# Optimization experiments

Measured on AMD Instinct MI355X. Metric: run time of the kernel, lower is better.

Reference implementation:

```python
import jax, jax.numpy as jnp
import numpy as np

B, S, D, H = 4, 2048, 1024, 16
HD = D // H

def setup_inputs() -> dict:
    key = jax.random.key(0)
    ks = jax.random.split(key, 9)
    s = 1.0 / np.sqrt(D)
    return {
        "x": jax.random.normal(ks[0], (B, S, D), dtype=jnp.float32),
        "wq": jax.random.normal(ks[1], (D, D), dtype=jnp.float32) * s,
        "bq": jnp.zeros((D,), dtype=jnp.float32),
        "wk": jax.random.normal(ks[2], (D, D), dtype=jnp.float32) * s,
        "bk": jnp.zeros((D,), dtype=jnp.float32),
        "wv": jax.random.normal(ks[3], (D, D), dtype=jnp.float32) * s,
        "bv": jnp.zeros((D,), dtype=jnp.float32),
        "wo": jax.random.normal(ks[4], (D, D), dtype=jnp.float32) * s,
        "bo": jnp.zeros((D,), dtype=jnp.float32),
    }

def reference(x, wq, bq, wk, bk, wv, bv, wo, bo):
    # QKV projections, split heads: [B,S,D] -> [B,H,S,HD]
    def split_heads(t):
        return t.reshape(B, S, H, HD).transpose(0, 2, 1, 3)
    q = split_heads(x @ wq + bq)
    k = split_heads(x @ wk + bk)
    v = split_heads(x @ wv + bv)
    # scaled dot-product attention with full score matrix [B,H,S,S]
    scores = jnp.einsum("bhqd,bhkd->bhqk", q, k) / jnp.sqrt(jnp.float32(HD))
    weights = jax.nn.softmax(scores, axis=-1)
    attn = jnp.einsum("bhqk,bhkd->bhqd", weights, v)
    # merge heads and output projection
    out = attn.transpose(0, 2, 1, 3).reshape(B, S, D) @ wo + bo
    return out
```

## Files before the change

kernel.cpp:

```cpp
#include <hip/hip_runtime.h>
#include <hip/hip_bf16.h>


#define B_  4
#define S_  2048
#define D_  1024
#define H_  16
#define HD_ 64
#define M_  (B_*S_)

typedef __attribute__((ext_vector_type(8))) short short8;
typedef __attribute__((ext_vector_type(4))) float f32x4;
typedef __hip_bfloat16 bf16;

__device__ inline void gload_lds16(const void* g, void* l) {
  __builtin_amdgcn_global_load_lds(
      (const __attribute__((address_space(1))) void*)g,
      (__attribute__((address_space(3))) void*)l,
      16, 0, 0);
}

__device__ inline f32x4 mfma16(short8 a, short8 b, f32x4 c) {
  return __builtin_amdgcn_mfma_f32_16x16x32_bf16(a, b, c, 0, 0, 0);
}

__device__ inline short bfbits(float f) {
  bf16 h = (bf16)f;
  return *reinterpret_cast<short*>(&h);
}

__global__ void convert_x_kernel(const float* __restrict__ x, bf16* __restrict__ xb) {
  const int i = (blockIdx.x * 256 + threadIdx.x) * 8;
  float4 a = *reinterpret_cast<const float4*>(x + i);
  float4 b = *reinterpret_cast<const float4*>(x + i + 4);
  bf16 o[8];
  o[0] = (bf16)a.x; o[1] = (bf16)a.y; o[2] = (bf16)a.z; o[3] = (bf16)a.w;
  o[4] = (bf16)b.x; o[5] = (bf16)b.y; o[6] = (bf16)b.z; o[7] = (bf16)b.w;
  *reinterpret_cast<int4*>(xb + i) = *reinterpret_cast<const int4*>(o);
}

struct TP { const float* w[4]; bf16* wt[4]; };

__global__ void transpose_w_kernel(TP p) {
  const float* w = p.w[blockIdx.z];
  bf16* wt = p.wt[blockIdx.z];
  __shared__ float t[32][33];
  const int k0 = blockIdx.y * 32, n0 = blockIdx.x * 32;
  const int c = threadIdx.x & 31, r4 = threadIdx.x >> 5;
  #pragma unroll
  for (int i = 0; i < 4; ++i) {
    int r = r4 + i * 8;
    t[r][c] = w[(size_t)(k0 + r) * D_ + n0 + c];
  }
  __syncthreads();
  #pragma unroll
  for (int i = 0; i < 4; ++i) {
    int r = r4 + i * 8;
    wt[(size_t)(n0 + r) * D_ + k0 + c] = (bf16)t[c][r];
  }
}

template<int MODE>
__global__ __launch_bounds__(256) void gemm_kernel(
    const bf16* __restrict__ A, const bf16* __restrict__ Bt,
    const float* __restrict__ bias, void* __restrict__ out, float alpha)
{
  constexpr int BK = 32;
  __shared__ __align__(16) bf16 As[128 * BK];
  __shared__ __align__(16) bf16 Bs[128 * BK];
  const int tid = threadIdx.x;
  const int w = tid >> 6, l = tid & 63;
  const int lo = l & 15, hi = l >> 4;
  const int wm = w >> 1, wn = w & 1;
  const int row0 = blockIdx.y * 128;
  const int col0 = blockIdx.x * 128;

  f32x4 acc[4][4] = {};

  for (int kt = 0; kt < D_; kt += BK) {
    __syncthreads();
    #pragma unroll
    for (int i = 0; i < 2; ++i) {
      const int cb = i * 256 + w * 64;
      const int c  = cb + l;
      gload_lds16(A  + (size_t)(row0 + (c >> 2)) * D_ + kt + (c & 3) * 8,
                  (void*)(As + cb * 8));
      gload_lds16(Bt + (size_t)(col0 + (c >> 2)) * D_ + kt + (c & 3) * 8,
                  (void*)(Bs + cb * 8));
    }
    __syncthreads();

    short8 a[4], b[4];
    #pragma unroll
    for (int m = 0; m < 4; ++m)
      a[m] = *reinterpret_cast<const short8*>(As + (wm*64 + m*16 + lo) * BK + hi*8);
    #pragma unroll
    for (int n = 0; n < 4; ++n)
      b[n] = *reinterpret_cast<const short8*>(Bs + (wn*64 + n*16 + lo) * BK + hi*8);
    #pragma unroll
    for (int m = 0; m < 4; ++m)
      #pragma unroll
      for (int n = 0; n < 4; ++n)
        acc[m][n] = mfma16(a[m], b[n], acc[m][n]);
  }

  #pragma unroll
  for (int n = 0; n < 4; ++n) {
    const int c = col0 + wn*64 + n*16 + lo;
    const float bv = bias[c];
    #pragma unroll
    for (int m = 0; m < 4; ++m) {
      #pragma unroll
      for (int j = 0; j < 4; ++j) {
        const int r = row0 + wm*64 + m*16 + hi*4 + j;
        const float v = (acc[m][n][j] + bv) * alpha;
        if (MODE == 2) {
          ((float*)out)[(size_t)r * D_ + c] = v;
        } else {
          const int bb = r >> 11, s = r & (S_ - 1);
          const int h = c >> 6, hd = c & 63;
          bf16* o = (bf16*)out;
          if (MODE == 0)
            o[((size_t)(bb * H_ + h) * S_ + s) * HD_ + hd] = (bf16)v;
          else
            o[((size_t)(bb * H_ + h) * HD_ + hd) * S_ + s] = (bf16)v;
        }
      }
    }
  }
}

__global__ __launch_bounds__(256, 2) void attn_kernel(
    const bf16* __restrict__ q, const bf16* __restrict__ k,
    const bf16* __restrict__ vt, bf16* __restrict__ ao)
{
  __shared__ __align__(16) bf16 Kl[64 * 72];
  __shared__ __align__(16) bf16 Vtl[64 * 72];

  const int tid = threadIdx.x;
  const int w = tid >> 6, l = tid & 63;
  const int lo = l & 15, hi = l >> 4;
  const int bh = blockIdx.y;
  const int q0 = blockIdx.x * 256 + w * 64;

  const bf16* kbase = k  + (size_t)bh * S_ * HD_;
  const bf16* vbase = vt + (size_t)bh * HD_ * S_;

  short8 bq[4][2];
  const size_t qrow = (size_t)bh * S_ + q0;
  #pragma unroll
  for (int n = 0; n < 4; ++n)
    #pragma unroll
    for (int kk = 0; kk < 2; ++kk)
      bq[n][kk] = *reinterpret_cast<const short8*>(
          q + (qrow + n*16 + lo) * HD_ + kk*32 + hi*8);

  f32x4 o[4][4] = {};
  float mrun[4], lrun[4];
  #pragma unroll
  for (int n = 0; n < 4; ++n) { mrun[n] = -3.0e38f; lrun[n] = 0.0f; }

  const int r0 = tid >> 3,        co0 = (tid & 7) * 8;
  const int r1 = (tid + 256) >> 3, co1 = (tid & 7) * 8;

  int4 kreg0, kreg1, vreg0, vreg1;
  kreg0 = *reinterpret_cast<const int4*>(kbase + (size_t)r0 * HD_ + co0);
  kreg1 = *reinterpret_cast<const int4*>(kbase + (size_t)r1 * HD_ + co1);
  vreg0 = *reinterpret_cast<const int4*>(vbase + (size_t)r0 * S_ + co0);
  vreg1 = *reinterpret_cast<const int4*>(vbase + (size_t)r1 * S_ + co1);

  for (int kt = 0; kt < S_; kt += 64) {
    __syncthreads();
    *reinterpret_cast<int4*>(Kl  + r0*72 + co0) = kreg0;
    *reinterpret_cast<int4*>(Kl  + r1*72 + co1) = kreg1;
    *reinterpret_cast<int4*>(Vtl + r0*72 + co0) = vreg0;
    *reinterpret_cast<int4*>(Vtl + r1*72 + co1) = vreg1;
    if (kt + 64 < S_) {
      const int nt = kt + 64;
      kreg0 = *reinterpret_cast<const int4*>(kbase + (size_t)(nt + r0) * HD_ + co0);
      kreg1 = *reinterpret_cast<const int4*>(kbase + (size_t)(nt + r1) * HD_ + co1);
      vreg0 = *reinterpret_cast<const int4*>(vbase + (size_t)r0 * S_ + nt + co0);
      vreg1 = *reinterpret_cast<const int4*>(vbase + (size_t)r1 * S_ + nt + co1);
    }
    __syncthreads();

    f32x4 s[4][4] = {};
    __builtin_amdgcn_s_setprio(1);
    #pragma unroll
    for (int m = 0; m < 4; ++m) {
      short8 kf0 = *reinterpret_cast<const short8*>(Kl + (m*16+lo)*72 + hi*8);
      short8 kf1 = *reinterpret_cast<const short8*>(Kl + (m*16+lo)*72 + 32 + hi*8);
      #pragma unroll
      for (int n = 0; n < 4; ++n) {
        s[m][n] = mfma16(kf0, bq[n][0], s[m][n]);
        s[m][n] = mfma16(kf1, bq[n][1], s[m][n]);
      }
    }
    __builtin_amdgcn_s_setprio(0);

    short8 pb[4][2];
    #pragma unroll
    for (int n = 0; n < 4; ++n) {
      float mx = fmaxf(
          fmaxf(fmaxf(fmaxf(s[0][n][0], s[0][n][1]), fmaxf(s[0][n][2], s[0][n][3])),
                fmaxf(fmaxf(s[1][n][0], s[1][n][1]), fmaxf(s[1][n][2], s[1][n][3]))),
          fmaxf(fmaxf(fmaxf(s[2][n][0], s[2][n][1]), fmaxf(s[2][n][2], s[2][n][3])),
                fmaxf(fmaxf(s[3][n][0], s[3][n][1]), fmaxf(s[3][n][2], s[3][n][3]))));
      mx = fmaxf(mx, __shfl_xor(mx, 16, 64));
      mx = fmaxf(mx, __shfl_xor(mx, 32, 64));
      const float mn = fmaxf(mrun[n], mx);
      const float corr = __expf(mrun[n] - mn);
      mrun[n] = mn;
      float sum = 0.0f;
      #pragma unroll
      for (int m = 0; m < 4; ++m)
        #pragma unroll
        for (int j = 0; j < 4; ++j) {
          const float p = __expf(s[m][n][j] - mn);
          s[m][n][j] = p;
          sum += p;
        }
      sum += __shfl_xor(sum, 16, 64);
      sum += __shfl_xor(sum, 32, 64);
      lrun[n] = lrun[n] * corr + sum;
      #pragma unroll
      for (int mm = 0; mm < 4; ++mm)
        #pragma unroll
        for (int j = 0; j < 4; ++j)
          o[mm][n][j] *= corr;
      #pragma unroll
      for (int kk = 0; kk < 2; ++kk) {
        short8 t;
        t[0] = bfbits(s[2*kk][n][0]);   t[1] = bfbits(s[2*kk][n][1]);
        t[2] = bfbits(s[2*kk][n][2]);   t[3] = bfbits(s[2*kk][n][3]);
        t[4] = bfbits(s[2*kk+1][n][0]); t[5] = bfbits(s[2*kk+1][n][1]);
        t[6] = bfbits(s[2*kk+1][n][2]); t[7] = bfbits(s[2*kk+1][n][3]);
        pb[n][kk] = t;
      }
    }

    __builtin_amdgcn_s_setprio(1);
    #pragma unroll
    for (int mm = 0; mm < 4; ++mm) {
      short8 vf[2];
      #pragma unroll
      for (int kk = 0; kk < 2; ++kk) {
        union { short8 v; uint2 u2[2]; } x;
        x.u2[0] = *reinterpret_cast<const uint2*>(Vtl + (mm*16+lo)*72 + kk*32 + hi*4);
        x.u2[1] = *reinterpret_cast<const uint2*>(Vtl + (mm*16+lo)*72 + kk*32 + 16 + hi*4);
        vf[kk] = x.v;
      }
      #pragma unroll
      for (int n = 0; n < 4; ++n) {
        o[mm][n] = mfma16(vf[0], pb[n][0], o[mm][n]);
        o[mm][n] = mfma16(vf[1], pb[n][1], o[mm][n]);
      }
    }
    __builtin_amdgcn_s_setprio(0);
  }

  const int b = bh >> 4, h = bh & 15;
  #pragma unroll
  for (int n = 0; n < 4; ++n) {
    const float inv = 1.0f / lrun[n];
    const size_t row = (size_t)b * S_ + q0 + n*16 + lo;
    #pragma unroll
    for (int mm = 0; mm < 4; ++mm) {
      bf16 ov[4];
      #pragma unroll
      for (int j = 0; j < 4; ++j) ov[j] = (bf16)(o[mm][n][j] * inv);
      *reinterpret_cast<uint2*>(ao + row * D_ + h*64 + mm*16 + hi*4) =
          *reinterpret_cast<const uint2*>(ov);
    }
  }
}

extern "C" void kernel_launch(void* const* d_in, const int* in_sizes, int n_in,
                              void* d_out, int out_size, void* d_ws, size_t ws_size,
                              hipStream_t stream) {
  const float* x  = (const float*)d_in[0];
  const float* wq = (const float*)d_in[1];
  const float* bq = (const float*)d_in[2];
  const float* wk = (const float*)d_in[3];
  const float* bk = (const float*)d_in[4];
  const float* wv = (const float*)d_in[5];
  const float* bv = (const float*)d_in[6];
  const float* wo = (const float*)d_in[7];
  const float* bo = (const float*)d_in[8];

  char* ws = (char*)d_ws;
  bf16* xb  = (bf16*)(ws);
  bf16* wqt = (bf16*)(ws + ((size_t)16 << 20));
  bf16* wkt = (bf16*)(ws + ((size_t)18 << 20));
  bf16* wvt = (bf16*)(ws + ((size_t)20 << 20));
  bf16* wot = (bf16*)(ws + ((size_t)22 << 20));
  bf16* qb  = (bf16*)(ws + ((size_t)24 << 20));
  bf16* kb  = (bf16*)(ws + ((size_t)40 << 20));
  bf16* vtb = (bf16*)(ws + ((size_t)56 << 20));
  bf16* aob = (bf16*)(ws + ((size_t)72 << 20));

  convert_x_kernel<<<dim3((M_ * D_) / (256 * 8)), 256, 0, stream>>>(x, xb);

  TP p;
  p.w[0] = wq; p.w[1] = wk; p.w[2] = wv; p.w[3] = wo;
  p.wt[0] = wqt; p.wt[1] = wkt; p.wt[2] = wvt; p.wt[3] = wot;
  transpose_w_kernel<<<dim3(32, 32, 4), 256, 0, stream>>>(p);

  dim3 ggrid(D_ / 128, M_ / 128);
  gemm_kernel<0><<<ggrid, 256, 0, stream>>>(xb, wqt, bq, qb, 0.125f);
  gemm_kernel<0><<<ggrid, 256, 0, stream>>>(xb, wkt, bk, kb, 1.0f);
  gemm_kernel<1><<<ggrid, 256, 0, stream>>>(xb, wvt, bv, vtb, 1.0f);

  attn_kernel<<<dim3(S_ / 256, B_ * H_), 256, 0, stream>>>(qb, kb, vtb, aob);

  gemm_kernel<2><<<ggrid, 256, 0, stream>>>(aob, wot, bo, d_out, 1.0f);
}
```

Baseline: 323.8 us.

## Fuse QKV GEMMs, shrink attention tiles, add lazy softmax rescale and exp2

Replaces the three separate Q/K/V projection GEMMs with one launch over the concatenated transposed weights, which happen to be laid out contiguously in the workspace. Each output column is routed to the Q, K or V layout in the epilogue. The attention kernel now gives each wave 32 query rows instead of 64, allows 4 blocks per CU, and remaps the flat block index to group blocks by head. It also folds log2(e) into the Q scale so it can use exp2, and skips the rescale of the output accumulator unless the running max grows by more than 8. The output GEMM uses 64-row tiles so the grid has more blocks. The costs are fewer MFMAs per K/V tile load, bounded growth of unnormalised probabilities, and a dependence on the workspace layout.

```diff
diff --git a/kernel.cpp b/kernel.cpp
--- a/kernel.cpp
+++ b/kernel.cpp
@@ -8,6 +8,7 @@
 #define H_  16
 #define HD_ 64
 #define M_  (B_*S_)
+#define QSCALE (0.125f * 1.4426950408889634f)
 
 typedef __attribute__((ext_vector_type(8))) short short8;
 typedef __attribute__((ext_vector_type(4))) float f32x4;
@@ -60,10 +61,11 @@
   }
 }
 
-template<int MODE>
-__global__ __launch_bounds__(256) void gemm_kernel(
-    const bf16* __restrict__ A, const bf16* __restrict__ Bt,
-    const float* __restrict__ bias, void* __restrict__ out, float alpha)
+__global__ __launch_bounds__(256) void gemm_qkv_kernel(
+    const bf16* __restrict__ A, const bf16* __restrict__ Bt3,
+    const float* __restrict__ bq, const float* __restrict__ bk,
+    const float* __restrict__ bv,
+    bf16* __restrict__ qb, bf16* __restrict__ kb, bf16* __restrict__ vtb)
 {
   constexpr int BK = 32;
   __shared__ __align__(16) bf16 As[128 * BK];
@@ -83,22 +85,94 @@
     for (int i = 0; i < 2; ++i) {
       const int cb = i * 256 + w * 64;
       const int c  = cb + l;
-      gload_lds16(A  + (size_t)(row0 + (c >> 2)) * D_ + kt + (c & 3) * 8,
+      gload_lds16(A   + (size_t)(row0 + (c >> 2)) * D_ + kt + (c & 3) * 8,
                   (void*)(As + cb * 8));
+      gload_lds16(Bt3 + (size_t)(col0 + (c >> 2)) * D_ + kt + (c & 3) * 8,
+                  (void*)(Bs + cb * 8));
+    }
+    __syncthreads();
+
+    short8 a[4], b[4];
+    #pragma unroll
+    for (int m = 0; m < 4; ++m)
+      a[m] = *reinterpret_cast<const short8*>(As + (wm*64 + m*16 + lo) * BK + hi*8);
+    #pragma unroll
+    for (int n = 0; n < 4; ++n)
+      b[n] = *reinterpret_cast<const short8*>(Bs + (wn*64 + n*16 + lo) * BK + hi*8);
+    #pragma unroll
+    for (int m = 0; m < 4; ++m)
+      #pragma unroll
+      for (int n = 0; n < 4; ++n)
+        acc[m][n] = mfma16(a[m], b[n], acc[m][n]);
+  }
+
+  #pragma unroll
+  for (int n = 0; n < 4; ++n) {
+    const int c3 = col0 + wn*64 + n*16 + lo;
+    const int which = c3 >> 10;
+    const int cc = c3 & 1023;
+    const int h = cc >> 6, hd = cc & 63;
+    const float* bias = (which == 0) ? bq : (which == 1) ? bk : bv;
+    const float bvv = bias[cc];
+    #pragma unroll
+    for (int m = 0; m < 4; ++m) {
+      #pragma unroll
+      for (int j = 0; j < 4; ++j) {
+        const int r = row0 + wm*64 + m*16 + hi*4 + j;
+        const int bb = r >> 11, s = r & (S_ - 1);
+        float v = acc[m][n][j] + bvv;
+        if (which == 0) {
+          v *= QSCALE;
+          qb[((size_t)(bb * H_ + h) * S_ + s) * HD_ + hd] = (bf16)v;
+        } else if (which == 1) {
+          kb[((size_t)(bb * H_ + h) * S_ + s) * HD_ + hd] = (bf16)v;
+        } else {
+          vtb[((size_t)(bb * H_ + h) * HD_ + hd) * S_ + s] = (bf16)v;
+        }
+      }
+    }
+  }
+}
+
+__global__ __launch_bounds__(256) void gemm_out_kernel(
+    const bf16* __restrict__ A, const bf16* __restrict__ Bt,
+    const float* __restrict__ bias, float* __restrict__ out)
+{
+  constexpr int BK = 32;
+  __shared__ __align__(16) bf16 As[64 * BK];
+  __shared__ __align__(16) bf16 Bs[128 * BK];
+  const int tid = threadIdx.x;
+  const int w = tid >> 6, l = tid & 63;
+  const int lo = l & 15, hi = l >> 4;
+  const int wm = w >> 1, wn = w & 1;
+  const int row0 = blockIdx.y * 64;
+  const int col0 = blockIdx.x * 128;
+
+  f32x4 acc[2][4] = {};
+
+  for (int kt = 0; kt < D_; kt += BK) {
+    __syncthreads();
+    #pragma unroll
+    for (int i = 0; i < 2; ++i) {
+      const int cb = i * 256 + w * 64;
+      const int c  = cb + l;
+      if (i == 0)
+        gload_lds16(A + (size_t)(row0 + (c >> 2)) * D_ + kt + (c & 3) * 8,
+                    (void*)(As + cb * 8));
       gload_lds16(Bt + (size_t)(col0 + (c >> 2)) * D_ + kt + (c & 3) * 8,
                   (void*)(Bs + cb * 8));
     }
     __syncthreads();
 
-    short8 a[4], b[4];
-    #pragma unroll
-    for (int m = 0; m < 4; ++m)
-      a[m] = *reinterpret_cast<const short8*>(As + (wm*64 + m*16 + lo) * BK + hi*8);
+    short8 a[2], b[4];
+    #pragma unroll
+    for (int m = 0; m < 2; ++m)
+      a[m] = *reinterpret_cast<const short8*>(As + (wm*32 + m*16 + lo) * BK + hi*8);
     #pragma unroll
     for (int n = 0; n < 4; ++n)
       b[n] = *reinterpret_cast<const short8*>(Bs + (wn*64 + n*16 + lo) * BK + hi*8);
     #pragma unroll
-    for (int m = 0; m < 4; ++m)
+    for (int m = 0; m < 2; ++m)
       #pragma unroll
       for (int n = 0; n < 4; ++n)
         acc[m][n] = mfma16(a[m], b[n], acc[m][n]);
@@ -107,30 +181,19 @@
   #pragma unroll
   for (int n = 0; n < 4; ++n) {
     const int c = col0 + wn*64 + n*16 + lo;
-    const float bv = bias[c];
-    #pragma unroll
-    for (int m = 0; m < 4; ++m) {
+    const float bvv = bias[c];
+    #pragma unroll
+    for (int m = 0; m < 2; ++m) {
       #pragma unroll
       for (int j = 0; j < 4; ++j) {
-        const int r = row0 + wm*64 + m*16 + hi*4 + j;
-        const float v = (acc[m][n][j] + bv) * alpha;
-        if (MODE == 2) {
-          ((float*)out)[(size_t)r * D_ + c] = v;
-        } else {
-          const int bb = r >> 11, s = r & (S_ - 1);
-          const int h = c >> 6, hd = c & 63;
-          bf16* o = (bf16*)out;
-          if (MODE == 0)
-            o[((size_t)(bb * H_ + h) * S_ + s) * HD_ + hd] = (bf16)v;
-          else
-            o[((size_t)(bb * H_ + h) * HD_ + hd) * S_ + s] = (bf16)v;
-        }
-      }
-    }
-  }
-}
-
-__global__ __launch_bounds__(256, 2) void attn_kernel(
+        const int r = row0 + wm*32 + m*16 + hi*4 + j;
+        out[(size_t)r * D_ + c] = acc[m][n][j] + bvv;
+      }
+    }
+  }
+}
+
+__global__ __launch_bounds__(256, 4) void attn_kernel(
     const bf16* __restrict__ q, const bf16* __restrict__ k,
     const bf16* __restrict__ vt, bf16* __restrict__ ao)
 {
@@ -140,27 +203,29 @@
   const int tid = threadIdx.x;
   const int w = tid >> 6, l = tid & 63;
   const int lo = l & 15, hi = l >> 4;
-  const int bh = blockIdx.y;
-  const int q0 = blockIdx.x * 256 + w * 64;
+  const int flat = blockIdx.x;
+  const int L = (flat & 7) * 128 + (flat >> 3);
+  const int bh = L >> 4;
+  const int q0 = (L & 15) * 128 + w * 32;
 
   const bf16* kbase = k  + (size_t)bh * S_ * HD_;
   const bf16* vbase = vt + (size_t)bh * HD_ * S_;
 
-  short8 bq[4][2];
+  short8 bq[2][2];
   const size_t qrow = (size_t)bh * S_ + q0;
   #pragma unroll
-  for (int n = 0; n < 4; ++n)
+  for (int n = 0; n < 2; ++n)
     #pragma unroll
     for (int kk = 0; kk < 2; ++kk)
       bq[n][kk] = *reinterpret_cast<const short8*>(
           q + (qrow + n*16 + lo) * HD_ + kk*32 + hi*8);
 
-  f32x4 o[4][4] = {};
-  float mrun[4], lrun[4];
-  #pragma unroll
-  for (int n = 0; n < 4; ++n) { mrun[n] = -3.0e38f; lrun[n] = 0.0f; }
-
-  const int r0 = tid >> 3,        co0 = (tid & 7) * 8;
+  f32x4 o[4][2] = {};
+  float mrun[2], lrun[2];
+  #pragma unroll
+  for (int n = 0; n < 2; ++n) { mrun[n] = -1.0e30f; lrun[n] = 0.0f; }
+
+  const int r0 = tid >> 3,         co0 = (tid & 7) * 8;
   const int r1 = (tid + 256) >> 3, co1 = (tid & 7) * 8;
 
   int4 kreg0, kreg1, vreg0, vreg1;
@@ -184,50 +249,58 @@
     }
     __syncthreads();
 
-    f32x4 s[4][4] = {};
+    f32x4 s[4][2] = {};
     __builtin_amdgcn_s_setprio(1);
     #pragma unroll
     for (int m = 0; m < 4; ++m) {
       short8 kf0 = *reinterpret_cast<const short8*>(Kl + (m*16+lo)*72 + hi*8);
       short8 kf1 = *reinterpret_cast<const short8*>(Kl + (m*16+lo)*72 + 32 + hi*8);
       #pragma unroll
-      for (int n = 0; n < 4; ++n) {
+      for (int n = 0; n < 2; ++n) {
         s[m][n] = mfma16(kf0, bq[n][0], s[m][n]);
         s[m][n] = mfma16(kf1, bq[n][1], s[m][n]);
       }
     }
     __builtin_amdgcn_s_setprio(0);
 
-    short8 pb[4][2];
-    #pragma unroll
-    for (int n = 0; n < 4; ++n) {
-      float mx = fmaxf(
-          fmaxf(fmaxf(fmaxf(s[0][n][0], s[0][n][1]), fmaxf(s[0][n][2], s[0][n][3])),
-                fmaxf(fmaxf(s[1][n][0], s[1][n][1]), fmaxf(s[1][n][2], s[1][n][3]))),
-          fmaxf(fmaxf(fmaxf(s[2][n][0], s[2][n][1]), fmaxf(s[2][n][2], s[2][n][3])),
-                fmaxf(fmaxf(s[3][n][0], s[3][n][1]), fmaxf(s[3][n][2], s[3][n][3]))));
+    short8 pb[2][2];
+    #pragma unroll
+    for (int n = 0; n < 2; ++n) {
+      float t0 = fmaxf(fmaxf(s[0][n][0], s[0][n][1]), s[0][n][2]);
+      float t1 = fmaxf(fmaxf(s[0][n][3], s[1][n][0]), s[1][n][1]);
+      float t2 = fmaxf(fmaxf(s[1][n][2], s[1][n][3]), s[2][n][0]);
+      float t3 = fmaxf(fmaxf(s[2][n][1], s[2][n][2]), s[2][n][3]);
+      float t4 = fmaxf(fmaxf(s[3][n][0], s[3][n][1]), s[3][n][2]);
+      float mx = fmaxf(fmaxf(fmaxf(t0, t1), fmaxf(t2, t3)),
+                       fmaxf(t4, s[3][n][3]));
       mx = fmaxf(mx, __shfl_xor(mx, 16, 64));
       mx = fmaxf(mx, __shfl_xor(mx, 32, 64));
-      const float mn = fmaxf(mrun[n], mx);
-      const float corr = __expf(mrun[n] - mn);
-      mrun[n] = mn;
+      float mn;
+      if (__all(mx <= mrun[n] + 8.0f)) {
+        mn = mrun[n];
+      } else {
+        mn = fmaxf(mrun[n], mx);
+        const float corr = exp2f(mrun[n] - mn);
+        lrun[n] *= corr;
+        #pragma unroll
+        for (int mm = 0; mm < 4; ++mm)
+          #pragma unroll
+          for (int j = 0; j < 4; ++j)
+            o[mm][n][j] *= corr;
+        mrun[n] = mn;
+      }
       float sum = 0.0f;
       #pragma unroll
       for (int m = 0; m < 4; ++m)
         #pragma unroll
         for (int j = 0; j < 4; ++j) {
-          const float p = __expf(s[m][n][j] - mn);
+          const float p = exp2f(s[m][n][j] - mn);
           s[m][n][j] = p;
           sum += p;
         }
       sum += __shfl_xor(sum, 16, 64);
       sum += __shfl_xor(sum, 32, 64);
-      lrun[n] = lrun[n] * corr + sum;
-      #pragma unroll
-      for (int mm = 0; mm < 4; ++mm)
-        #pragma unroll
-        for (int j = 0; j < 4; ++j)
-          o[mm][n][j] *= corr;
+      lrun[n] += sum;
       #pragma unroll
       for (int kk = 0; kk < 2; ++kk) {
         short8 t;
@@ -251,7 +324,7 @@
         vf[kk] = x.v;
       }
       #pragma unroll
-      for (int n = 0; n < 4; ++n) {
+      for (int n = 0; n < 2; ++n) {
         o[mm][n] = mfma16(vf[0], pb[n][0], o[mm][n]);
         o[mm][n] = mfma16(vf[1], pb[n][1], o[mm][n]);
       }
@@ -261,7 +334,7 @@
 
   const int b = bh >> 4, h = bh & 15;
   #pragma unroll
-  for (int n = 0; n < 4; ++n) {
+  for (int n = 0; n < 2; ++n) {
     const float inv = 1.0f / lrun[n];
     const size_t row = (size_t)b * S_ + q0 + n*16 + lo;
     #pragma unroll
@@ -306,12 +379,10 @@
   p.wt[0] = wqt; p.wt[1] = wkt; p.wt[2] = wvt; p.wt[3] = wot;
   transpose_w_kernel<<<dim3(32, 32, 4), 256, 0, stream>>>(p);
 
-  dim3 ggrid(D_ / 128, M_ / 128);
-  gemm_kernel<0><<<ggrid, 256, 0, stream>>>(xb, wqt, bq, qb, 0.125f);
-  gemm_kernel<0><<<ggrid, 256, 0, stream>>>(xb, wkt, bk, kb, 1.0f);
-  gemm_kernel<1><<<ggrid, 256, 0, stream>>>(xb, wvt, bv, vtb, 1.0f);
-
-  attn_kernel<<<dim3(S_ / 256, B_ * H_), 256, 0, stream>>>(qb, kb, vtb, aob);
-
-  gemm_kernel<2><<<ggrid, 256, 0, stream>>>(aob, wot, bo, d_out, 1.0f);
-}
+  gemm_qkv_kernel<<<dim3(24, 64), 256, 0, stream>>>(
+      xb, wqt, bq, bk, bv, qb, kb, vtb);
+
+  attn_kernel<<<dim3(1024), 256, 0, stream>>>(qb, kb, vtb, aob);
+
+  gemm_out_kernel<<<dim3(8, 128), 256, 0, stream>>>(aob, wot, bo, (float*)d_out);
+}
```

New measurement: 340.5 us. 5.2% more time.
